# Performance work log

Measured on AMD Instinct MI355X. Metric: run time of the kernel, lower is better.

## Reference

```python
import jax, jax.numpy as jnp
import numpy as np

B, C, H, W = 32, 256, 32, 32


def setup_inputs() -> dict:
    key = jax.random.key(0)
    k1, k2, k3 = jax.random.split(key, 3)
    h = jax.random.normal(k1, (B, C, H, W), dtype=jnp.float32)
    w1_w = jax.random.normal(k2, (1, C), dtype=jnp.float32) * (1.0 / np.sqrt(C))
    w1_b = jnp.zeros((1,), dtype=jnp.float32)
    w2_w = jax.random.normal(k3, (1, C), dtype=jnp.float32) * (1.0 / np.sqrt(C))
    w2_b = jnp.zeros((1,), dtype=jnp.float32)
    return {"h": h, "w1_w": w1_w, "w1_b": w1_b, "w2_w": w2_w, "w2_b": w2_b}


def reference(h, w1_w, w1_b, w2_w, w2_b):
    b, c, hh, ww = h.shape
    x = jnp.transpose(h, (0, 2, 3, 1))            # [B,H,W,C]
    # scalar projections of every spatial token
    a = jnp.einsum('bhwc,c->bhw', x, w1_w[0]) + w1_b[0]   # query-side scalar [B,H,W]
    k = jnp.einsum('bhwc,c->bhw', x, w2_w[0]) + w2_b[0]   # key-side scalar   [B,H,W]
    n = hh * ww
    # additive attention scores over all spatial pairs: [B,H,W,HW]
    scores = jnp.tanh(a[:, :, :, None] + k.reshape(b, 1, 1, n))
    attn = jax.nn.softmax(scores, axis=-1)                 # exp(tanh)/sum == softmax(tanh)
    ctx = jnp.einsum('bijn,bnc->bijc', attn, x.reshape(b, n, c))  # [B,H,W,C]
    out = jnp.where(ctx >= 0, ctx, 0.2 * ctx)              # LeakyReLU(0.2)
    return jnp.transpose(out, (0, 3, 1, 2))                # [B,C,H,W]
```

## Files before the change

kernel.cpp:

```cpp
#include <hip/hip_runtime.h>

constexpr int Bn = 32;
constexpr int Cn = 256;
constexpr int Nn = 1024;

constexpr float C2 = 2.8853900817779268f;
constexpr float K1 = 1.4426950408889634f;

typedef __bf16 v8bf  __attribute__((ext_vector_type(8)));
typedef float  v16f  __attribute__((ext_vector_type(16)));


__global__ __launch_bounds__(512) void prep_kernel(
    const float* __restrict__ h,
    const float* __restrict__ w1, const float* __restrict__ w1b,
    const float* __restrict__ w2, const float* __restrict__ w2b,
    float* __restrict__ pa_g, float* __restrict__ q_g,
    unsigned char* __restrict__ hbf)
{
    int blk = blockIdx.x;
    int xcd = blk & 7, idx = blk >> 3;
    int b   = xcd * 4 + (idx >> 4);
    int n0  = (idx & 15) * 64;
    int t = threadIdx.x, w = t >> 6, l = t & 63;

    __shared__ float lds_t[128][68];
    __shared__ float p1[8][64], p2[8][64];

    const float* hb = h + (size_t)b * Cn * Nn + n0;
    float s1 = 0.f, s2 = 0.f;

    int ccP   = (w >> 2) * 64 + l;
    int ntl   = (w >> 1) & 1;
    int gbase = (w & 1) * 2;
    int nt32  = (n0 >> 5) + ntl;
    unsigned char* nt_base = hbf + (size_t)(b * 32 + nt32) * 16384;

    for (int chunk = 0; chunk < 2; ++chunk) {
        if (chunk) __syncthreads();
#pragma unroll 8
        for (int ci = 0; ci < 16; ++ci) {
            int cc = w * 16 + ci;
            int c  = chunk * 128 + cc;
            float v = hb[(size_t)c * Nn + l];
            s1 = fmaf(v, w1[c], s1);
            s2 = fmaf(v, w2[c], s2);
            lds_t[cc][l] = v;
        }
        __syncthreads();
        int c = chunk * 128 + ccP;
        unsigned char* crow = nt_base + c * 64;
#pragma unroll
        for (int g2 = 0; g2 < 2; ++g2) {
            int g   = gbase + g2;
            int col = ntl * 32 + g * 8;
            float4 va = *(const float4*)&lds_t[ccP][col];
            float4 vb = *(const float4*)&lds_t[ccP][col + 4];
            union { __bf16 bx[8]; uint4 u4; } pk;
            pk.bx[0] = (__bf16)va.x; pk.bx[1] = (__bf16)va.y;
            pk.bx[2] = (__bf16)va.z; pk.bx[3] = (__bf16)va.w;
            pk.bx[4] = (__bf16)vb.x; pk.bx[5] = (__bf16)vb.y;
            pk.bx[6] = (__bf16)vb.z; pk.bx[7] = (__bf16)vb.w;
            *(uint4*)(crow + ((g ^ (c & 3)) << 4)) = pk.u4;
        }
    }

    p1[w][l] = s1;
    p2[w][l] = s2;
    __syncthreads();
    if (t < 64) {
        float a = w1b[0], k = w2b[0];
#pragma unroll
        for (int ww = 0; ww < 8; ++ww) { a += p1[ww][t]; k += p2[ww][t]; }
        pa_g[b * Nn + n0 + t] = exp2f(C2 * a);
        q_g [b * Nn + n0 + t] = exp2f(C2 * k);
    }
}

constexpr int EST_OFF  = 0;
constexpr int QS_OFF   = 16384;
constexpr int SP_OFF   = 65792;
constexpr int SINV_OFF = 67840;
constexpr int CTX_SMEM = 68096;

__global__ __launch_bounds__(512, 4) void ctx_kernel(
    const unsigned char* __restrict__ hbf,
    const float* __restrict__ pa_g, const float* __restrict__ q_g,
    float* __restrict__ out)
{
    __shared__ alignas(16) unsigned char smem[CTX_SMEM];
    float* qs           = (float*)(smem + QS_OFF);
    float (*Sp)[64]     = (float(*)[64])(smem + SP_OFF);
    float* Sinv         = (float*)(smem + SINV_OFF);
    float (*comb)[257]  = (float(*)[257])smem;

    int blk = blockIdx.x;
    int xcd = blk & 7, slot = blk >> 3;
    int b   = xcd * 4 + (slot >> 4);
    int i0  = (slot & 15) * 64;

    int t = threadIdx.x, w = t >> 6, l = t & 63;
    int lm = l & 31, lh = l >> 5;
    int cq = w & 3, wq = w >> 2;

    const unsigned char* hbf_b = hbf + (size_t)b * 524288;

    for (int i = t; i < Nn; i += 512) qs[i] = q_g[b * Nn + i];
    float pav = pa_g[b * Nn + i0 + l];

    v16f acc[2][2];
#pragma unroll
    for (int x = 0; x < 2; ++x)
#pragma unroll
        for (int y = 0; y < 2; ++y)
#pragma unroll
            for (int r = 0; r < 16; ++r) acc[x][y][r] = 0.f;
    float Spart = 0.f;

    int est_sw = l * 128 + ((w ^ (l & 7)) << 4);

    int cB   = cq * 64 + lm;
    int m4   = cB & 3;
    int off0 = cB * 64 + ((lh ^ m4) << 4);
    int off1 = cB * 64 + (((2 + lh) ^ m4) << 4);

    __syncthreads();
    for (int tt = 0; tt < 16; ++tt) {
        unsigned char* est_base = smem + EST_OFF + ((tt & 1) << 13);
        const unsigned char* pt = hbf_b + (size_t)((wq << 4) + tt) * 16384;
        v8bf b00 = *(const v8bf*)(pt + off0);
        v8bf b01 = *(const v8bf*)(pt + off0 + 2048);
        v8bf b10 = *(const v8bf*)(pt + off1);
        v8bf b11 = *(const v8bf*)(pt + off1 + 2048);
        {
            int qb = wq * 512 + tt * 32 + cq * 8;
            float4 q0 = *(const float4*)&qs[qb];
            float4 q1 = *(const float4*)&qs[qb + 4];
            float qv[8] = {q0.x, q0.y, q0.z, q0.w, q1.x, q1.y, q1.z, q1.w};
            v8bf ev;
#pragma unroll
            for (int j = 0; j < 8; ++j) {
                float z = pav * qv[j];
                float r = __builtin_amdgcn_rcpf(1.f + z);
                float e = exp2f(fmaf(r, -2.f * K1, K1));
                __bf16 eb = (__bf16)e;
                ev[j] = eb;
                Spart += (float)eb;
            }
            *(v8bf*)(est_base + est_sw) = ev;
        }
        __syncthreads();
#pragma unroll
        for (int ks = 0; ks < 2; ++ks) {
            int gA = ((wq << 2) + (ks << 1) + lh) ^ (lm & 7);
            v8bf a0 = *(const v8bf*)(est_base + lm * 128        + (gA << 4));
            v8bf a1 = *(const v8bf*)(est_base + (32 + lm) * 128 + (gA << 4));
            v8bf b0 = ks ? b10 : b00;
            v8bf b1 = ks ? b11 : b01;
            acc[0][0] = __builtin_amdgcn_mfma_f32_32x32x16_bf16(a0, b0, acc[0][0], 0, 0, 0);
            acc[0][1] = __builtin_amdgcn_mfma_f32_32x32x16_bf16(a0, b1, acc[0][1], 0, 0, 0);
            acc[1][0] = __builtin_amdgcn_mfma_f32_32x32x16_bf16(a1, b0, acc[1][0], 0, 0, 0);
            acc[1][1] = __builtin_amdgcn_mfma_f32_32x32x16_bf16(a1, b1, acc[1][1], 0, 0, 0);
        }
    }

    Sp[w][l] = Spart;
    __syncthreads();
    if (t < 64) {
        float S = 0.f;
#pragma unroll
        for (int ww = 0; ww < 8; ++ww) S += Sp[ww][t];
        Sinv[t] = 1.f / S;
    }
    if (wq == 1) {
#pragma unroll
        for (int x = 0; x < 2; ++x)
#pragma unroll
            for (int y = 0; y < 2; ++y)
#pragma unroll
                for (int r = 0; r < 16; ++r) {
                    int rl = (r & 3) + 8 * (r >> 2) + 4 * lh;
                    comb[x * 32 + rl][cq * 64 + y * 32 + lm] = acc[x][y][r];
                }
    }
    __syncthreads();
    if (wq == 0) {
#pragma unroll
        for (int x = 0; x < 2; ++x)
#pragma unroll
            for (int y = 0; y < 2; ++y)
#pragma unroll
                for (int r = 0; r < 16; ++r) {
                    int rl  = (r & 3) + 8 * (r >> 2) + 4 * lh;
                    int row = x * 32 + rl;
                    int col = cq * 64 + y * 32 + lm;
                    float v = (acc[x][y][r] + comb[row][col]) * Sinv[row];
                    v = (v >= 0.f) ? v : 0.2f * v;
                    comb[row][col] = v;
                }
    }
    __syncthreads();
    float* ob = out + (size_t)b * Cn * Nn + i0;
#pragma unroll
    for (int p = 0; p < 8; ++p) {
        int slot = t + (p << 9);
        int c    = slot >> 4;
        int i4   = (slot & 15) << 2;
        float4 o;
        o.x = comb[i4 + 0][c];
        o.y = comb[i4 + 1][c];
        o.z = comb[i4 + 2][c];
        o.w = comb[i4 + 3][c];
        *(float4*)(ob + (size_t)c * Nn + i4) = o;
    }
}

extern "C" void kernel_launch(void* const* d_in, const int* in_sizes, int n_in,
                              void* d_out, int out_size, void* d_ws, size_t ws_size,
                              hipStream_t stream) {
    const float* h   = (const float*)d_in[0];
    const float* w1w = (const float*)d_in[1];
    const float* w1b = (const float*)d_in[2];
    const float* w2w = (const float*)d_in[3];
    const float* w2b = (const float*)d_in[4];
    float* out = (float*)d_out;

    float* pa_ws = (float*)d_ws;
    float* q_ws  = pa_ws + Bn * Nn;
    unsigned char* hbf = (unsigned char*)d_ws + 262144;

    prep_kernel<<<512, 512, 0, stream>>>(h, w1w, w1b, w2w, w2b, pa_ws, q_ws, hbf);
    ctx_kernel <<<512, 512, 0, stream>>>(hbf, pa_ws, q_ws, out);
}
```

Baseline: 119.3 us.

## Drop LDS transpose in prep kernel; load 8 contiguous tokens per thread with shuffle reductions

The prep kernel no longer stages h through a shared-memory tile before converting it to bf16. Each thread now loads eight contiguous spatial values of one channel with float4 loads, packs them into bf16, and writes them straight to the swizzled layout. The two dot-product sums are kept per token and reduced with cross-lane xor shuffles. This removes the LDS round trip and the barriers between the two chunks, but adds register pressure and shuffle work, and each load instruction now covers fewer distinct channel rows.

Result: no change. 120.1 us (+0.7%).

```diff
diff --git a/kernel.cpp b/kernel.cpp
--- a/kernel.cpp
+++ b/kernel.cpp
@@ -23,50 +23,52 @@
     int b   = xcd * 4 + (idx >> 4);
     int n0  = (idx & 15) * 64;
     int t = threadIdx.x, w = t >> 6, l = t & 63;
-
-    __shared__ float lds_t[128][68];
+    int co = l >> 3, oct = l & 7;
+
     __shared__ float p1[8][64], p2[8][64];
 
-    const float* hb = h + (size_t)b * Cn * Nn + n0;
-    float s1 = 0.f, s2 = 0.f;
-
-    int ccP   = (w >> 2) * 64 + l;
-    int ntl   = (w >> 1) & 1;
-    int gbase = (w & 1) * 2;
-    int nt32  = (n0 >> 5) + ntl;
+    float s1[8], s2[8];
+#pragma unroll
+    for (int j = 0; j < 8; ++j) { s1[j] = 0.f; s2[j] = 0.f; }
+
+    const float* hb = h + (size_t)b * Cn * Nn + n0 + oct * 8;
+    int nt32 = (n0 >> 5) + (oct >> 2);
     unsigned char* nt_base = hbf + (size_t)(b * 32 + nt32) * 16384;
-
-    for (int chunk = 0; chunk < 2; ++chunk) {
-        if (chunk) __syncthreads();
-#pragma unroll 8
-        for (int ci = 0; ci < 16; ++ci) {
-            int cc = w * 16 + ci;
-            int c  = chunk * 128 + cc;
-            float v = hb[(size_t)c * Nn + l];
-            s1 = fmaf(v, w1[c], s1);
-            s2 = fmaf(v, w2[c], s2);
-            lds_t[cc][l] = v;
-        }
-        __syncthreads();
-        int c = chunk * 128 + ccP;
-        unsigned char* crow = nt_base + c * 64;
-#pragma unroll
-        for (int g2 = 0; g2 < 2; ++g2) {
-            int g   = gbase + g2;
-            int col = ntl * 32 + g * 8;
-            float4 va = *(const float4*)&lds_t[ccP][col];
-            float4 vb = *(const float4*)&lds_t[ccP][col + 4];
-            union { __bf16 bx[8]; uint4 u4; } pk;
-            pk.bx[0] = (__bf16)va.x; pk.bx[1] = (__bf16)va.y;
-            pk.bx[2] = (__bf16)va.z; pk.bx[3] = (__bf16)va.w;
-            pk.bx[4] = (__bf16)vb.x; pk.bx[5] = (__bf16)vb.y;
-            pk.bx[6] = (__bf16)vb.z; pk.bx[7] = (__bf16)vb.w;
-            *(uint4*)(crow + ((g ^ (c & 3)) << 4)) = pk.u4;
-        }
-    }
-
-    p1[w][l] = s1;
-    p2[w][l] = s2;
+    int g = oct & 3;
+
+#pragma unroll
+    for (int it = 0; it < 4; ++it) {
+        int c = it * 64 + w * 8 + co;
+        const float* src = hb + (size_t)c * Nn;
+        float4 va = *(const float4*)src;
+        float4 vb = *(const float4*)(src + 4);
+        float w1c = w1[c], w2c = w2[c];
+        float v[8] = {va.x, va.y, va.z, va.w, vb.x, vb.y, vb.z, vb.w};
+        union { __bf16 bx[8]; uint4 u4; } pk;
+#pragma unroll
+        for (int j = 0; j < 8; ++j) {
+            s1[j] = fmaf(v[j], w1c, s1[j]);
+            s2[j] = fmaf(v[j], w2c, s2[j]);
+            pk.bx[j] = (__bf16)v[j];
+        }
+        *(uint4*)(nt_base + c * 64 + ((g ^ (c & 3)) << 4)) = pk.u4;
+    }
+
+#pragma unroll
+    for (int m = 8; m <= 32; m <<= 1) {
+#pragma unroll
+        for (int j = 0; j < 8; ++j) {
+            s1[j] += __shfl_xor(s1[j], m);
+            s2[j] += __shfl_xor(s2[j], m);
+        }
+    }
+    if (co == 0) {
+#pragma unroll
+        for (int j = 0; j < 8; ++j) {
+            p1[w][oct * 8 + j] = s1[j];
+            p2[w][oct * 8 + j] = s2[j];
+        }
+    }
     __syncthreads();
     if (t < 64) {
         float a = w1b[0], k = w2b[0];
```
